# Kernel optimization log

Measured on AMD Instinct MI355X. Metric: run time of the kernel, lower is better.

## Reference

```python
import jax, jax.numpy as jnp
import numpy as np

B, QL, KVL = 2, 1024, 2048
D = 4096          # hidden_size
NH, NKV = 32, 8   # attention heads / kv heads
HD = D // NH      # head_dim = 128
INNER = 4 * D     # SwiGLU intermediate = 16384
EPS = 1e-5
THETA = 10000.0


def rope_cos_sin(seq_len, head_dim, theta):
    inv_freq = 1.0 / (theta ** (jnp.arange(0, head_dim, 2, dtype=jnp.float32) / head_dim))
    t = jnp.arange(seq_len, dtype=jnp.float32)
    freqs = jnp.outer(t, inv_freq)                      # [S, HD/2]
    emb = jnp.concatenate([freqs, freqs], axis=-1)      # [S, HD]
    return jnp.cos(emb), jnp.sin(emb)


def rotate_half(x):
    half = x.shape[-1] // 2
    return jnp.concatenate([-x[..., half:], x[..., :half]], axis=-1)


def apply_rope(x, cos, sin):
    # x: [B, H, S, HD]; cos/sin: [S, HD] broadcast over batch & heads
    return x * cos[None, None] + rotate_half(x) * sin[None, None]


def layernorm(x, w, b):
    mu = jnp.mean(x, axis=-1, keepdims=True)
    var = jnp.var(x, axis=-1, keepdims=True)
    return (x - mu) * jax.lax.rsqrt(var + EPS) * w + b


def setup_inputs() -> dict:
    key = jax.random.key(0)
    ks = jax.random.split(key, 12)
    s = 0.02
    return {
        "hidden_states": jax.random.normal(ks[0], (B, QL, D), jnp.float32),
        "encoder_hidden_states": jax.random.normal(ks[1], (B, KVL, D), jnp.float32),
        "encoder_attention_mask": jnp.ones((B, KVL), jnp.float32),
        "ln1_w": jnp.ones((D,), jnp.float32),
        "ln1_b": jnp.zeros((D,), jnp.float32),
        "q_w": jax.random.normal(ks[2], (D, D), jnp.float32) * s,        # [out, in]
        "k_w": jax.random.normal(ks[3], (NKV * HD, D), jnp.float32) * s,
        "v_w": jax.random.normal(ks[4], (NKV * HD, D), jnp.float32) * s,
        "o_w": jax.random.normal(ks[5], (D, D), jnp.float32) * s,
        "ln2_w": jnp.ones((D,), jnp.float32),
        "ln2_b": jnp.zeros((D,), jnp.float32),
        "gate_w": jax.random.normal(ks[6], (INNER, D), jnp.float32) * s,
        "up_w": jax.random.normal(ks[7], (INNER, D), jnp.float32) * s,
        "down_w": jax.random.normal(ks[8], (D, INNER), jnp.float32) * s,
    }


def reference(hidden_states, encoder_hidden_states, encoder_attention_mask,
              ln1_w, ln1_b, q_w, k_w, v_w, o_w, ln2_w, ln2_b,
              gate_w, up_w, down_w):
    residual = hidden_states
    h = layernorm(hidden_states, ln1_w, ln1_b)

    # projections
    q = (h @ q_w.T).reshape(B, QL, NH, HD).transpose(0, 2, 1, 3)                    # [B,NH,QL,HD]
    k = (encoder_hidden_states @ k_w.T).reshape(B, KVL, NKV, HD).transpose(0, 2, 1, 3)  # [B,NKV,KVL,HD]
    v = (encoder_hidden_states @ v_w.T).reshape(B, KVL, NKV, HD).transpose(0, 2, 1, 3)

    # RoPE: q uses positions 0..QL-1, k uses positions 0..KVL-1 (position_ids=None -> cos[None])
    q_cos, q_sin = rope_cos_sin(QL, HD, THETA)
    kv_cos, kv_sin = rope_cos_sin(KVL, HD, THETA)
    q = apply_rope(q, q_cos, q_sin)
    k = apply_rope(k, kv_cos, kv_sin)

    # GQA repeat_kv: each kv head repeated num_key_value_groups times consecutively
    n_rep = NH // NKV
    k = jnp.repeat(k, n_rep, axis=1)  # [B,NH,KVL,HD]
    v = jnp.repeat(v, n_rep, axis=1)

    attn = jnp.einsum('bhqd,bhkd->bhqk', q, k) / np.sqrt(HD).astype(np.float32)
    # NOTE: original code ADDS the boolean mask (True -> +1.0) to the logits
    mask = (encoder_attention_mask != 0).astype(attn.dtype)  # [B,KVL]
    attn = attn + mask[:, None, None, :]
    attn = jax.nn.softmax(attn.astype(jnp.float32), axis=-1).astype(q.dtype)

    out = jnp.einsum('bhqk,bhkd->bhqd', attn, v)        # [B,NH,QL,HD]
    out = out.transpose(0, 2, 1, 3).reshape(B, QL, D)
    attn_out = out @ o_w.T

    h = residual + attn_out
    residual = h
    h = layernorm(h, ln2_w, ln2_b)
    ff = (jax.nn.silu(h @ gate_w.T) * (h @ up_w.T)) @ down_w.T
    return residual + ff
```

## Files before the change

kernel.cpp:

```cpp
#include <hip/hip_runtime.h>
#include <hip/hip_bf16.h>
#include <math.h>

using bf16 = __hip_bfloat16;
typedef __bf16 bfv8 __attribute__((ext_vector_type(8)));
typedef float f32x4 __attribute__((ext_vector_type(4)));

__device__ __forceinline__ f32x4 mfma16(bfv8 a, bfv8 b, f32x4 c) {
    return __builtin_amdgcn_mfma_f32_16x16x32_bf16(a, b, c, 0, 0, 0);
}

__device__ __forceinline__ void gload_lds16(const void* g, void* l) {
    __builtin_amdgcn_global_load_lds(
        (const __attribute__((address_space(1))) void*)g,
        (__attribute__((address_space(3))) void*)l, 16, 0, 0);
}

__global__ void cvt_kernel(const float* __restrict__ in, bf16* __restrict__ out, long n8) {
    long u = (long)blockIdx.x * 256 + threadIdx.x;
    if (u >= n8) return;
    const float4* p = (const float4*)in + u * 2;
    float4 a = p[0], b = p[1];
    bf16 t8[8] = { __float2bfloat16(a.x), __float2bfloat16(a.y), __float2bfloat16(a.z), __float2bfloat16(a.w),
                   __float2bfloat16(b.x), __float2bfloat16(b.y), __float2bfloat16(b.z), __float2bfloat16(b.w) };
    *(int4*)(out + u * 8) = *(const int4*)t8;
}

__global__ void cvt2_kernel(const float* __restrict__ in1, bf16* __restrict__ out1,
                            const float* __restrict__ in2, bf16* __restrict__ out2, long n8) {
    long u = (long)blockIdx.x * 256 + threadIdx.x;
    const float* in = in1;
    bf16* out = out1;
    if (u >= n8) { u -= n8; in = in2; out = out2; }
    const float4* p = (const float4*)in + u * 2;
    float4 a = p[0], b = p[1];
    bf16 t8[8] = { __float2bfloat16(a.x), __float2bfloat16(a.y), __float2bfloat16(a.z), __float2bfloat16(a.w),
                   __float2bfloat16(b.x), __float2bfloat16(b.y), __float2bfloat16(b.z), __float2bfloat16(b.w) };
    *(int4*)(out + u * 8) = *(const int4*)t8;
}

__global__ void layernorm_kernel(const float* __restrict__ x, const float* __restrict__ gw,
                                 const float* __restrict__ gb, bf16* __restrict__ out)
{
    const int D = 4096;
    int row = blockIdx.x, t = threadIdx.x;
    const float4* xr = (const float4*)(x + (size_t)row * D);
    float4 v[4];
    float s1 = 0.f, s2 = 0.f;
#pragma unroll
    for (int j = 0; j < 4; ++j) {
        v[j] = xr[t + j * 256];
        s1 += v[j].x + v[j].y + v[j].z + v[j].w;
        s2 += v[j].x * v[j].x + v[j].y * v[j].y + v[j].z * v[j].z + v[j].w * v[j].w;
    }
#pragma unroll
    for (int d = 1; d < 64; d <<= 1) { s1 += __shfl_xor(s1, d); s2 += __shfl_xor(s2, d); }
    __shared__ float red[8];
    int wave = t >> 6, lane = t & 63;
    if (lane == 0) { red[wave] = s1; red[4 + wave] = s2; }
    __syncthreads();
    s1 = red[0] + red[1] + red[2] + red[3];
    s2 = red[4] + red[5] + red[6] + red[7];
    float mu = s1 * (1.f / 4096.f);
    float var = s2 * (1.f / 4096.f) - mu * mu;
    float rs = rsqrtf(var + 1e-5f);
    bf16* orow = out + (size_t)row * D;
#pragma unroll
    for (int j = 0; j < 4; ++j) {
        int base = (t + j * 256) * 4;
        float xs[4] = { v[j].x, v[j].y, v[j].z, v[j].w };
        bf16 o4[4];
#pragma unroll
        for (int c = 0; c < 4; ++c)
            o4[c] = __float2bfloat16((xs[c] - mu) * rs * gw[base + c] + gb[base + c]);
        *(int2*)(orow + base) = *(const int2*)o4;
    }
}

__global__ void rope_kernel(bf16* __restrict__ x, int nheads, int seqlen, long total) {
    long idx = (long)blockIdx.x * 256 + threadIdx.x;
    if (idx >= total) return;
    int j = (int)(idx & 63);
    long t2 = idx >> 6;
    int h = (int)(t2 % nheads);
    long row = t2 / nheads;
    int pos = (int)(row % seqlen);
    float inv = exp2f(-(float)j * 0.20762050593046015f);
    float ang = (float)pos * inv;
    float s, c;
    sincosf(ang, &s, &c);
    bf16* p = x + row * ((long)nheads * 128) + (long)h * 128 + j;
    float x0 = __bfloat162float(p[0]);
    float x1 = __bfloat162float(p[64]);
    p[0]  = __float2bfloat16(x0 * c - x1 * s);
    p[64] = __float2bfloat16(x1 * c + x0 * s);
}

template<int BM, int BN, int MODE, bool DUAL, int CM, int CN, int XN>
__global__ __launch_bounds__(512, 2) void gemm_p(
        const bf16* __restrict__ A, const bf16* __restrict__ W, const bf16* __restrict__ W2,
        void* __restrict__ Cout, void* __restrict__ Cout2, const void* __restrict__ aux,
        int M, int N, int K, int Nsplit)
{
    constexpr int MF = BM / 32;
    constexpr int NF = BN / 64;
    constexpr int ALD = BM / 128;
    constexpr int BLD = BN / 128;
    constexpr int SLD = ALD + BLD;
    __shared__ bf16 lds[3][(BM + BN) * 32];

    const int t = threadIdx.x;
    const int wid = t >> 6, lane = t & 63;
    const int lr = lane & 15, lg = lane >> 4;
    const int wr = wid >> 2, wc = wid & 3;
    const int bid = blockIdx.x;
    const int xcd = bid & 7, slot = bid >> 3;
    const int sm = slot / CN, sn = slot % CN;
    const int xm = xcd / XN, xn = xcd % XN;
    const int bm = (xm * CM + sm) * BM;
    const int bn = (xn * CN + sn) * BN;

    auto stage = [&](int tt, int buf) {
        const int k0 = tt * 32;
        char* ldsA = (char*)&lds[buf][0];
#pragma unroll
        for (int c = 0; c < ALD; ++c) {
            int Wb = (t + c * 512) * 16;
            int L = Wb ^ (((Wb >> 7) & 7) << 4);
            int row = L >> 6, colb = L & 63;
            gload_lds16(A + (size_t)(bm + row) * K + k0 + (colb >> 1), ldsA + Wb);
        }
        char* ldsB = (char*)&lds[buf][BM * 32];
#pragma unroll
        for (int c = 0; c < BLD; ++c) {
            int Wb = (t + c * 512) * 16;
            int L = Wb ^ (((Wb >> 7) & 7) << 4);
            int row = L >> 6, colb = L & 63;
            const bf16* src;
            if constexpr (DUAL) {
                int nr = bn + row;
                src = (nr >= Nsplit) ? W2 + (size_t)(nr - Nsplit) * K + k0 + (colb >> 1)
                                     : W  + (size_t)nr * K + k0 + (colb >> 1);
            } else {
                src = W + (size_t)(bn + row) * K + k0 + (colb >> 1);
            }
            gload_lds16(src, ldsB + Wb);
        }
    };

    const f32x4 zero4 = { 0.f, 0.f, 0.f, 0.f };
    f32x4 acc[MF][NF];
#pragma unroll
    for (int m = 0; m < MF; ++m)
#pragma unroll
        for (int n = 0; n < NF; ++n) acc[m][n] = zero4;

    const int T = K >> 5;
    stage(0, 0);
    stage(1, 1);
    if constexpr (SLD == 4) asm volatile("s_waitcnt vmcnt(4)" ::: "memory");
    else                    asm volatile("s_waitcnt vmcnt(3)" ::: "memory");
    __builtin_amdgcn_s_barrier();
    __builtin_amdgcn_sched_barrier(0);

    for (int tt = 0; tt < T; ++tt) {
        const int buf = tt % 3;
        bfv8 af[MF], bfr[NF];
#pragma unroll
        for (int m = 0; m < MF; ++m) {
            int row = wr * (BM / 2) + m * 16 + lr;
            int U = row * 64 + lg * 16;
            af[m] = *(const bfv8*)((const char*)&lds[buf][0] + (U ^ (((U >> 7) & 7) << 4)));
        }
#pragma unroll
        for (int n = 0; n < NF; ++n) {
            int row = wc * (BN / 4) + n * 16 + lr;
            int U = row * 64 + lg * 16;
            bfr[n] = *(const bfv8*)((const char*)&lds[buf][BM * 32] + (U ^ (((U >> 7) & 7) << 4)));
        }
        if (tt + 2 < T) stage(tt + 2, (tt + 2) % 3);
        __builtin_amdgcn_s_setprio(1);
#pragma unroll
        for (int m = 0; m < MF; ++m)
#pragma unroll
            for (int n = 0; n < NF; ++n)
                acc[m][n] = mfma16(af[m], bfr[n], acc[m][n]);
        __builtin_amdgcn_s_setprio(0);
        if (tt + 2 < T) {
            if constexpr (SLD == 4) asm volatile("s_waitcnt vmcnt(4)" ::: "memory");
            else                    asm volatile("s_waitcnt vmcnt(3)" ::: "memory");
        } else {
            asm volatile("s_waitcnt vmcnt(0)" ::: "memory");
        }
        __builtin_amdgcn_s_barrier();
        __builtin_amdgcn_sched_barrier(0);
    }

    const int r0 = bm + wr * (BM / 2), c0 = bn + wc * (BN / 4);
#pragma unroll
    for (int m = 0; m < MF; ++m)
#pragma unroll
        for (int n = 0; n < NF; ++n)
#pragma unroll
            for (int i = 0; i < 4; ++i) {
                int r = r0 + m * 16 + lg * 4 + i;
                int c = c0 + n * 16 + lr;
                float a = acc[m][n][i];
                if constexpr (DUAL) {
                    if (c < Nsplit) ((bf16*)Cout)[(size_t)r * Nsplit + c] = __float2bfloat16(a);
                    else ((bf16*)Cout2)[(size_t)r * (N - Nsplit) + (c - Nsplit)] = __float2bfloat16(a);
                } else {
                    size_t idx = (size_t)r * N + c;
                    if constexpr (MODE == 0) {
                        ((bf16*)Cout)[idx] = __float2bfloat16(a);
                    } else if constexpr (MODE == 1) {
                        a = a / (1.f + expf(-a));
                        ((bf16*)Cout)[idx] = __float2bfloat16(a);
                    } else if constexpr (MODE == 2) {
                        a *= __bfloat162float(((const bf16*)aux)[idx]);
                        ((bf16*)Cout)[idx] = __float2bfloat16(a);
                    } else {
                        ((float*)Cout)[idx] = a + ((const float*)aux)[idx];
                    }
                }
            }
}

template<int BN, int MODE, bool DUAL, int CM, int CN, int XN>
__global__ __launch_bounds__(512, 1) void gemm8(
        const bf16* __restrict__ A, const bf16* __restrict__ W, const bf16* __restrict__ W2,
        void* __restrict__ Cout, void* __restrict__ Cout2, const void* __restrict__ aux,
        int M, int N, int K, int Nsplit)
{
    constexpr bool BIG = (BN == 256);
    constexpr int NBUF = BIG ? 2 : 3;
    constexpr int ABY = 32768;
    constexpr int BBY = BN * 128;
    constexpr int TBY = ABY + BBY;
    __shared__ alignas(16) char lds8[NBUF * TBY];

    const int t = threadIdx.x;
    const int wid = t >> 6, lane = t & 63;
    const int lr = lane & 15, lg = lane >> 4;
    const int wrB = wid >> 2, wcB = wid & 3;
    const int wr4 = wid >> 1, wc4 = wid & 1;
    const int bid = blockIdx.x;
    const int xcd = bid & 7, slot = bid >> 3;
    const int sm = slot / CN, sn = slot % CN;
    const int xm = xcd / XN, xn = xcd % XN;
    const int bm = (xm * CM + sm) * 256;
    const int bn = (xn * CN + sn) * BN;

    auto stA = [&](int kt, int h, int buf) {
#pragma unroll
        for (int c = 0; c < 2; ++c) {
            int Wb = (t + c * 512) * 16;
            int L = Wb ^ (((Wb >> 7) & 7) << 4);
            gload_lds16(A + (size_t)(bm + h * 128 + (L >> 7)) * K + kt * 64 + ((L & 127) >> 1),
                        lds8 + buf * TBY + h * 16384 + Wb);
        }
    };
    auto stB = [&](int kt, int h, int buf) {
#pragma unroll
        for (int c = 0; c < 2; ++c) {
            int Wb = (t + c * 512) * 16;
            int L = Wb ^ (((Wb >> 7) & 7) << 4);
            int nr = bn + h * 128 + (L >> 7);
            const bf16* src;
            if constexpr (DUAL) {
                src = (nr >= Nsplit) ? W2 + (size_t)(nr - Nsplit) * K + kt * 64 + ((L & 127) >> 1)
                                     : W  + (size_t)nr * K + kt * 64 + ((L & 127) >> 1);
            } else {
                src = W + (size_t)nr * K + kt * 64 + ((L & 127) >> 1);
            }
            gload_lds16(src, lds8 + buf * TBY + ABY + h * 16384 + Wb);
        }
    };

    const f32x4 zero4 = { 0.f, 0.f, 0.f, 0.f };
    f32x4 acc[BIG ? 8 : 4][4];
#pragma unroll
    for (int m = 0; m < (BIG ? 8 : 4); ++m)
#pragma unroll
        for (int n = 0; n < 4; ++n) acc[m][n] = zero4;

    bfv8 af[4][2], bfr[2][2][2];
    bfv8 afs[2][2], bfs[4][2];

#define LOADA(BUF, MH) do {                                                   \
    const char* _ba = lds8 + (BUF) * TBY;                                     \
    _Pragma("unroll") for (int m = 0; m < 4; ++m)                             \
    _Pragma("unroll") for (int ks = 0; ks < 2; ++ks) {                        \
        int row = wrB * 128 + (MH) * 64 + m * 16 + lr;                        \
        int U = row * 128 + ks * 64 + lg * 16;                                \
        af[m][ks] = *(const bfv8*)(_ba + (U ^ ((row & 7) << 4)));             \
    } } while (0)

#define LOADB(BUF, NH) do {                                                   \
    const char* _bb = lds8 + (BUF) * TBY + ABY;                               \
    _Pragma("unroll") for (int n = 0; n < 2; ++n)                             \
    _Pragma("unroll") for (int ks = 0; ks < 2; ++ks) {                        \
        int row = wcB * 64 + (NH) * 32 + n * 16 + lr;                         \
        int U = row * 128 + ks * 64 + lg * 16;                                \
        bfr[NH][n][ks] = *(const bfv8*)(_bb + (U ^ ((row & 7) << 4)));        \
    } } while (0)

#define MFMAQ(MH, NH) do {                                                    \
    _Pragma("unroll") for (int m = 0; m < 4; ++m)                             \
    _Pragma("unroll") for (int n = 0; n < 2; ++n) {                           \
        acc[(MH)*4+m][(NH)*2+n] = mfma16(af[m][0], bfr[NH][n][0], acc[(MH)*4+m][(NH)*2+n]); \
        acc[(MH)*4+m][(NH)*2+n] = mfma16(af[m][1], bfr[NH][n][1], acc[(MH)*4+m][(NH)*2+n]); \
    } } while (0)

#define LOADA_S(BUF, MH) do {                                                 \
    const char* _ba = lds8 + (BUF) * TBY;                                     \
    _Pragma("unroll") for (int m = 0; m < 2; ++m)                             \
    _Pragma("unroll") for (int ks = 0; ks < 2; ++ks) {                        \
        int row = wr4 * 64 + (MH) * 32 + m * 16 + lr;                         \
        int U = row * 128 + ks * 64 + lg * 16;                                \
        afs[m][ks] = *(const bfv8*)(_ba + (U ^ ((row & 7) << 4)));            \
    } } while (0)

#define LOADB_S(BUF) do {                                                     \
    const char* _bb = lds8 + (BUF) * TBY + ABY;                               \
    _Pragma("unroll") for (int n = 0; n < 4; ++n)                             \
    _Pragma("unroll") for (int ks = 0; ks < 2; ++ks) {                        \
        int row = wc4 * 64 + n * 16 + lr;                                     \
        int U = row * 128 + ks * 64 + lg * 16;                                \
        bfs[n][ks] = *(const bfv8*)(_bb + (U ^ ((row & 7) << 4)));            \
    } } while (0)

#define MFMAQ_S(MH) do {                                                      \
    _Pragma("unroll") for (int m = 0; m < 2; ++m)                             \
    _Pragma("unroll") for (int n = 0; n < 4; ++n) {                           \
        acc[(MH)*2+m][n] = mfma16(afs[m][0], bfs[n][0], acc[(MH)*2+m][n]);    \
        acc[(MH)*2+m][n] = mfma16(afs[m][1], bfs[n][1], acc[(MH)*2+m][n]);    \
    } } while (0)

#define PH_TOP() do { __builtin_amdgcn_s_barrier();                           \
    asm volatile("s_waitcnt lgkmcnt(0)" ::: "memory");                        \
    __builtin_amdgcn_sched_barrier(0);                                        \
    __builtin_amdgcn_s_setprio(1); } while (0)

#define PH_END() do { __builtin_amdgcn_s_setprio(0);                          \
    __builtin_amdgcn_s_barrier(); } while (0)

#define GATE(LIVE) do { __builtin_amdgcn_s_setprio(0);                        \
    if (LIVE) { if constexpr (BIG) asm volatile("s_waitcnt vmcnt(4)" ::: "memory"); \
                else               asm volatile("s_waitcnt vmcnt(6)" ::: "memory"); } \
    else      asm volatile("s_waitcnt vmcnt(0)" ::: "memory");                \
    __builtin_amdgcn_s_barrier(); } while (0)

    const int T = K >> 6;
    const int T2 = T >> 1;

    if constexpr (BIG) {
        stA(0, 0, 0); stA(0, 1, 0); stB(0, 0, 0); stB(0, 1, 0);
        stB(1, 0, 1); stB(1, 1, 1);
        asm volatile("s_waitcnt vmcnt(4)" ::: "memory");
        __builtin_amdgcn_s_barrier();

        for (int tt = 0; tt < T2; ++tt) {
            const int o = 2 * tt + 1, e2 = 2 * tt + 2, o2 = 2 * tt + 3;
            const bool le = (e2 < T), lo = (o2 < T);
            LOADA(0, 0); LOADB(0, 0); stA(o, 0, 1);
            PH_TOP(); MFMAQ(0, 0); PH_END();
            LOADB(0, 1); stA(o, 1, 1);
            PH_TOP(); MFMAQ(0, 1); PH_END();
            LOADA(0, 1); if (le) stB(e2, 0, 0);
            PH_TOP(); MFMAQ(1, 1); PH_END();
            if (le) stB(e2, 1, 0);
            PH_TOP(); MFMAQ(1, 0); GATE(le);
            LOADA(1, 0); LOADB(1, 0); if (le) stA(e2, 0, 0);
            PH_TOP(); MFMAQ(0, 0); PH_END();
            LOADB(1, 1); if (le) stA(e2, 1, 0);
            PH_TOP(); MFMAQ(0, 1); PH_END();
            LOADA(1, 1); if (lo) stB(o2, 0, 1);
            PH_TOP(); MFMAQ(1, 1); PH_END();
            if (lo) stB(o2, 1, 1);
            PH_TOP(); MFMAQ(1, 0); GATE(le);
        }
    } else {
        stA(0, 0, 0); stB(0, 0, 0); stA(0, 1, 0);
        stA(1, 0, 1); stB(1, 0, 1); stA(1, 1, 1);
        asm volatile("s_waitcnt vmcnt(6)" ::: "memory");
        __builtin_amdgcn_s_barrier();

        int bE = 0, bO = 1, bN = 2;
        for (int tt = 0; tt < T2; ++tt) {
            const int e2 = 2 * tt + 2, o2 = 2 * tt + 3;
            const bool le = (e2 < T), lo = (o2 < T);
            LOADA_S(bE, 0); LOADB_S(bE); if (le) { stA(e2, 0, bN); stB(e2, 0, bN); }
            PH_TOP(); MFMAQ_S(0); PH_END();
            LOADA_S(bE, 1); if (le) stA(e2, 1, bN);
            PH_TOP(); MFMAQ_S(1); GATE(le);
            LOADA_S(bO, 0); LOADB_S(bO); if (lo) { stA(o2, 0, bE); stB(o2, 0, bE); }
            PH_TOP(); MFMAQ_S(0); PH_END();
            LOADA_S(bO, 1); if (lo) stA(o2, 1, bE);
            PH_TOP(); MFMAQ_S(1); GATE(lo);
            int nE = bN, nO = bE, nN = bO;
            bE = nE; bO = nO; bN = nN;
        }
    }

#undef LOADA
#undef LOADB
#undef MFMAQ
#undef LOADA_S
#undef LOADB_S
#undef MFMAQ_S
#undef PH_TOP
#undef PH_END
#undef GATE

    const int r0 = bm + (BIG ? wrB * 128 : wr4 * 64);
    const int c0 = bn + (BIG ? wcB * 64 : wc4 * 64);
#pragma unroll
    for (int mg = 0; mg < (BIG ? 8 : 4); ++mg)
#pragma unroll
        for (int ng = 0; ng < 4; ++ng)
#pragma unroll
            for (int i = 0; i < 4; ++i) {
                int r = r0 + mg * 16 + lg * 4 + i;
                int c = c0 + ng * 16 + lr;
                float a = acc[mg][ng][i];
                if constexpr (DUAL) {
                    if (c < Nsplit) ((bf16*)Cout)[(size_t)r * Nsplit + c] = __float2bfloat16(a);
                    else ((bf16*)Cout2)[(size_t)r * (N - Nsplit) + (c - Nsplit)] = __float2bfloat16(a);
                } else {
                    size_t idx = (size_t)r * N + c;
                    if constexpr (MODE == 0) {
                        ((bf16*)Cout)[idx] = __float2bfloat16(a);
                    } else if constexpr (MODE == 1) {
                        a = a / (1.f + expf(-a));
                        ((bf16*)Cout)[idx] = __float2bfloat16(a);
                    } else if constexpr (MODE == 2) {
                        a *= __bfloat162float(((const bf16*)aux)[idx]);
                        ((bf16*)Cout)[idx] = __float2bfloat16(a);
                    } else {
                        ((float*)Cout)[idx] = a + ((const float*)aux)[idx];
                    }
                }
            }
}

__global__ void transpose_v(const bf16* __restrict__ vb, bf16* __restrict__ vt) {
    __shared__ bf16 tile[64][68];
    int kv0 = blockIdx.x * 64, c0 = blockIdx.y * 64, b = blockIdx.z;
    int t = threadIdx.x;
    int cr = t & 15, rr = t >> 4;
#pragma unroll
    for (int j = 0; j < 4; ++j) {
        int r = rr + j * 16;
        *(int2*)&tile[r][cr * 4] = *(const int2*)&vb[(size_t)(b * 2048 + kv0 + r) * 1024 + c0 + cr * 4];
    }
    __syncthreads();
#pragma unroll
    for (int j = 0; j < 4; ++j) {
        int cc = rr + j * 16;
        bf16 tmp[4];
#pragma unroll
        for (int q = 0; q < 4; ++q) tmp[q] = tile[cr * 4 + q][cc];
        *(int2*)&vt[(size_t)(b * 1024 + c0 + cc) * 2048 + kv0 + cr * 4] = *(const int2*)tmp;
    }
}

__global__ __launch_bounds__(256) void attn_kernel(
    const bf16* __restrict__ Q, const bf16* __restrict__ Kb, const bf16* __restrict__ Vt,
    const float* __restrict__ mask, bf16* __restrict__ O)
{
    const int QL_ = 1024, KVL_ = 2048;
    const float scale = 0.08838834764831845f;
    int qt = blockIdx.x, h = blockIdx.y, b = blockIdx.z;
    int t = threadIdx.x, wave = t >> 6, lane = t & 63;
    int lr = lane & 15, lg = lane >> 4;
    int g = h >> 2;
    __shared__ bf16 Ksm[2][64 * 128];
    __shared__ bf16 Vsm[2][128 * 64];
    __shared__ bf16 Psm[4][16 * 72];
    int q0 = qt * 64 + wave * 16;

    auto stage = [&](int buf, int kv0) {
#pragma unroll
        for (int p2 = 0; p2 < 4; ++p2) {
            int Wb = (p2 * 256 + t) * 16;
            int row = Wb >> 8;
            int col = ((Wb & 255) ^ ((row & 7) << 4)) >> 1;
            gload_lds16(Kb + (size_t)(b * KVL_ + kv0 + row) * 1024 + g * 128 + col,
                        (char*)&Ksm[buf][0] + Wb);
        }
#pragma unroll
        for (int p2 = 0; p2 < 4; ++p2) {
            int Wb = (p2 * 256 + t) * 16;
            int row = Wb >> 7;
            int col = ((Wb & 127) ^ ((row & 7) << 4)) >> 1;
            gload_lds16(Vt + (size_t)(b * 1024 + g * 128 + row) * 2048 + kv0 + col,
                        (char*)&Vsm[buf][0] + Wb);
        }
    };

    const bf16* qptr = Q + (size_t)(b * QL_ + q0 + lr) * 4096 + h * 128;
    bfv8 qf[4];
#pragma unroll
    for (int kc = 0; kc < 4; ++kc) qf[kc] = *(const bfv8*)(qptr + kc * 32 + lg * 8);

    const f32x4 zero4 = { 0.f, 0.f, 0.f, 0.f };
    f32x4 accO[8];
#pragma unroll
    for (int dt = 0; dt < 8; ++dt) accO[dt] = zero4;
    float mrow[4] = { -1e30f, -1e30f, -1e30f, -1e30f };
    float lrow[4] = { 0.f, 0.f, 0.f, 0.f };

    stage(0, 0);
    int buf = 0;
    const int NT = KVL_ / 64;
    for (int tt = 0; tt < NT; ++tt) {
        const int kv0 = tt * 64;
        if (tt + 1 < NT) {
            stage(buf ^ 1, kv0 + 64);
            asm volatile("s_waitcnt vmcnt(8)" ::: "memory");
        } else {
            asm volatile("s_waitcnt vmcnt(0)" ::: "memory");
        }
        __builtin_amdgcn_s_barrier();

        f32x4 s[4];
#pragma unroll
        for (int ct = 0; ct < 4; ++ct) {
            s[ct] = zero4;
#pragma unroll
            for (int kc = 0; kc < 4; ++kc) {
                int row = ct * 16 + lr;
                int U = row * 256 + kc * 64 + lg * 16;
                bfv8 kf = *(const bfv8*)((const char*)&Ksm[buf][0] + (U ^ ((row & 7) << 4)));
                s[ct] = mfma16(qf[kc], kf, s[ct]);
            }
            float mv = mask[(size_t)b * KVL_ + kv0 + ct * 16 + lr];
            mv = (mv != 0.f) ? 1.f : 0.f;
#pragma unroll
            for (int i = 0; i < 4; ++i) s[ct][i] = s[ct][i] * scale + mv;
        }

        float rmx[4], mnew[4], corr[4], psum[4];
#pragma unroll
        for (int i = 0; i < 4; ++i) {
            rmx[i] = fmaxf(fmaxf(s[0][i], s[1][i]), fmaxf(s[2][i], s[3][i]));
#pragma unroll
            for (int d = 1; d < 16; d <<= 1) rmx[i] = fmaxf(rmx[i], __shfl_xor(rmx[i], d));
            mnew[i] = fmaxf(mrow[i], rmx[i]);
            corr[i] = expf(mrow[i] - mnew[i]);
            psum[i] = 0.f;
        }
#pragma unroll
        for (int ct = 0; ct < 4; ++ct)
#pragma unroll
            for (int i = 0; i < 4; ++i) {
                float pv = expf(s[ct][i] - mnew[i]);
                psum[i] += pv;
                Psm[wave][(lg * 4 + i) * 72 + ct * 16 + lr] = __float2bfloat16(pv);
            }
#pragma unroll
        for (int i = 0; i < 4; ++i) {
#pragma unroll
            for (int d = 1; d < 16; d <<= 1) psum[i] += __shfl_xor(psum[i], d);
            lrow[i] = lrow[i] * corr[i] + psum[i];
            mrow[i] = mnew[i];
        }
#pragma unroll
        for (int dt = 0; dt < 8; ++dt)
#pragma unroll
            for (int i = 0; i < 4; ++i) accO[dt][i] *= corr[i];

        bfv8 pf0 = *(const bfv8*)&Psm[wave][lr * 72 + 0 * 32 + lg * 8];
        bfv8 pf1 = *(const bfv8*)&Psm[wave][lr * 72 + 1 * 32 + lg * 8];
#pragma unroll
        for (int dt = 0; dt < 8; ++dt) {
            int row = dt * 16 + lr;
            int U0 = row * 128 + 0 * 64 + lg * 16;
            int U1 = row * 128 + 1 * 64 + lg * 16;
            bfv8 vf0 = *(const bfv8*)((const char*)&Vsm[buf][0] + (U0 ^ ((row & 7) << 4)));
            bfv8 vf1 = *(const bfv8*)((const char*)&Vsm[buf][0] + (U1 ^ ((row & 7) << 4)));
            accO[dt] = mfma16(pf0, vf0, accO[dt]);
            accO[dt] = mfma16(pf1, vf1, accO[dt]);
        }
        __builtin_amdgcn_s_barrier();
        buf ^= 1;
    }

    float invl[4];
#pragma unroll
    for (int i = 0; i < 4; ++i) invl[i] = 1.f / lrow[i];
#pragma unroll
    for (int dt = 0; dt < 8; ++dt)
#pragma unroll
        for (int i = 0; i < 4; ++i)
            O[(size_t)(b * QL_ + q0 + lg * 4 + i) * 4096 + h * 128 + dt * 16 + lr] =
                __float2bfloat16(accO[dt][i] * invl[i]);
}

extern "C" void kernel_launch(void* const* d_in, const int* in_sizes, int n_in,
                              void* d_out, int out_size, void* d_ws, size_t ws_size,
                              hipStream_t stream) {
    const float* hidden = (const float*)d_in[0];
    const float* enc    = (const float*)d_in[1];
    const float* mask   = (const float*)d_in[2];
    const float* ln1w   = (const float*)d_in[3];
    const float* ln1b   = (const float*)d_in[4];
    const float* qw     = (const float*)d_in[5];
    const float* kw     = (const float*)d_in[6];
    const float* vw     = (const float*)d_in[7];
    const float* ow     = (const float*)d_in[8];
    const float* ln2w   = (const float*)d_in[9];
    const float* ln2b   = (const float*)d_in[10];
    const float* gatew  = (const float*)d_in[11];
    const float* upw    = (const float*)d_in[12];
    const float* downw  = (const float*)d_in[13];
    float* out = (float*)d_out;
    char* ws = (char*)d_ws;

    bf16*  wbuf  = (bf16*)(ws);
    bf16*  wbuf2 = (bf16*)(ws + 8388608);
    bf16*  h1    = (bf16*)(ws + 134217728);
    bf16*  encb  = (bf16*)(ws + 150994944);
    bf16*  qb    = (bf16*)(ws + 184549376);
    bf16*  kb    = (bf16*)(ws + 201326592);
    bf16*  vb    = (bf16*)(ws + 209715200);
    bf16*  attno = (bf16*)(ws + 218103808);
    float* h2    = (float*)(ws + 234881024);
    bf16*  vt    = (bf16*)(ws + 234881024);
    bf16*  h2n   = (bf16*)(ws + 268435456);
    bf16*  g1    = (bf16*)(ws + 285212672);

    auto cvt = [&](const float* src, bf16* dst, long n) {
        cvt_kernel<<<(int)(n / 2048), 256, 0, stream>>>(src, dst, n / 8);
    };

    cvt(enc, encb, 16777216L);
    layernorm_kernel<<<2048, 256, 0, stream>>>(hidden, ln1w, ln1b, h1);

    cvt(qw, wbuf, 16777216L);
    gemm_p<128, 256, 0, false, 8, 4, 4><<<256, 512, 0, stream>>>(
        h1, wbuf, nullptr, qb, nullptr, nullptr, 2048, 4096, 4096, 0);
    rope_kernel<<<16384, 256, 0, stream>>>(qb, 32, 1024, 2048L * 32 * 64);

    cvt2_kernel<<<4096, 256, 0, stream>>>(kw, wbuf, vw, wbuf2, 524288L);
    gemm_p<128, 256, 0, true, 8, 4, 2><<<256, 512, 0, stream>>>(
        encb, wbuf, wbuf2, kb, vb, nullptr, 4096, 2048, 4096, 1024);
    rope_kernel<<<8192, 256, 0, stream>>>(kb, 8, 2048, 4096L * 8 * 64);
    transpose_v<<<dim3(32, 16, 2), 256, 0, stream>>>(vb, vt);

    attn_kernel<<<dim3(16, 32, 2), 256, 0, stream>>>(qb, kb, vt, mask, attno);

    cvt(ow, wbuf, 16777216L);
    gemm_p<128, 256, 3, false, 8, 4, 4><<<256, 512, 0, stream>>>(
        attno, wbuf, nullptr, h2, nullptr, hidden, 2048, 4096, 4096, 0);

    layernorm_kernel<<<2048, 256, 0, stream>>>(h2, ln2w, ln2b, h2n);

    cvt(gatew, wbuf, 67108864L);
    gemm8<256, 1, false, 8, 8, 8><<<512, 512, 0, stream>>>(
        h2n, wbuf, nullptr, g1, nullptr, nullptr, 2048, 16384, 4096, 0);
    cvt(upw, wbuf, 67108864L);
    gemm8<256, 2, false, 8, 8, 8><<<512, 512, 0, stream>>>(
        h2n, wbuf, nullptr, g1, nullptr, g1, 2048, 16384, 4096, 0);

    cvt(downw, wbuf, 67108864L);
    gemm8<128, 3, false, 8, 4, 8><<<256, 512, 0, stream>>>(
        g1, wbuf, nullptr, out, nullptr, h2, 2048, 4096, 16384, 0);
}
```

Baseline: 1.504 ms.

## Overlap weight fp32-to-bf16 conversions with GEMMs via extra converter blocks

Extends the projection GEMM kernel with extra blocks beyond the GEMM grid that convert upcoming weights (K/V, gate) from fp32 to bf16 while the GEMM tiles run, and merges the encoder and Q-weight conversions into one launch. A larger workspace layout keeps separate buffers so these conversions can run ahead without clobbering live data. The aim is to hide the memory-bound conversion passes and cut launch count. The converter blocks compete with GEMM blocks for CUs and bandwidth, and the path needs a larger workspace, falling back to the old schedule otherwise.

```diff
diff --git a/kernel.cpp b/kernel.cpp
--- a/kernel.cpp
+++ b/kernel.cpp
@@ -100,8 +100,30 @@
 __global__ __launch_bounds__(512, 2) void gemm_p(
         const bf16* __restrict__ A, const bf16* __restrict__ W, const bf16* __restrict__ W2,
         void* __restrict__ Cout, void* __restrict__ Cout2, const void* __restrict__ aux,
-        int M, int N, int K, int Nsplit)
+        int M, int N, int K, int Nsplit,
+        int ngemm, const float* __restrict__ cf1, bf16* __restrict__ cd1, long cn1,
+        const float* __restrict__ cf2, bf16* __restrict__ cd2, long cn2)
 {
+    const int t = threadIdx.x;
+    if ((int)blockIdx.x >= ngemm) {
+        const long nb = (long)gridDim.x - ngemm;
+        const long tot = cn1 + cn2;
+        for (long u = (long)((int)blockIdx.x - ngemm) * 512 + t; u < tot; u += nb * 512) {
+            const float* in = cf1;
+            bf16* op = cd1;
+            long v = u;
+            if (v >= cn1) { v -= cn1; in = cf2; op = cd2; }
+            float4 a = ((const float4*)in)[v * 2];
+            float4 b = ((const float4*)in)[v * 2 + 1];
+            bf16 t8[8] = { __float2bfloat16(a.x), __float2bfloat16(a.y),
+                           __float2bfloat16(a.z), __float2bfloat16(a.w),
+                           __float2bfloat16(b.x), __float2bfloat16(b.y),
+                           __float2bfloat16(b.z), __float2bfloat16(b.w) };
+            *(int4*)(op + v * 8) = *(const int4*)t8;
+        }
+        return;
+    }
+
     constexpr int MF = BM / 32;
     constexpr int NF = BN / 64;
     constexpr int ALD = BM / 128;
@@ -109,7 +131,6 @@
     constexpr int SLD = ALD + BLD;
     __shared__ bf16 lds[3][(BM + BN) * 32];
 
-    const int t = threadIdx.x;
     const int wid = t >> 6, lane = t & 63;
     const int lr = lane & 15, lg = lane >> 4;
     const int wr = wid >> 2, wc = wid & 3;
@@ -618,53 +639,107 @@
     float* out = (float*)d_out;
     char* ws = (char*)d_ws;
 
-    bf16*  wbuf  = (bf16*)(ws);
-    bf16*  wbuf2 = (bf16*)(ws + 8388608);
-    bf16*  h1    = (bf16*)(ws + 134217728);
-    bf16*  encb  = (bf16*)(ws + 150994944);
-    bf16*  qb    = (bf16*)(ws + 184549376);
-    bf16*  kb    = (bf16*)(ws + 201326592);
-    bf16*  vb    = (bf16*)(ws + 209715200);
-    bf16*  attno = (bf16*)(ws + 218103808);
-    float* h2    = (float*)(ws + 234881024);
-    bf16*  vt    = (bf16*)(ws + 234881024);
-    bf16*  h2n   = (bf16*)(ws + 268435456);
-    bf16*  g1    = (bf16*)(ws + 285212672);
-
     auto cvt = [&](const float* src, bf16* dst, long n) {
         cvt_kernel<<<(int)(n / 2048), 256, 0, stream>>>(src, dst, n / 8);
     };
 
-    cvt(enc, encb, 16777216L);
-    layernorm_kernel<<<2048, 256, 0, stream>>>(hidden, ln1w, ln1b, h1);
-
-    cvt(qw, wbuf, 16777216L);
-    gemm_p<128, 256, 0, false, 8, 4, 4><<<256, 512, 0, stream>>>(
-        h1, wbuf, nullptr, qb, nullptr, nullptr, 2048, 4096, 4096, 0);
-    rope_kernel<<<16384, 256, 0, stream>>>(qb, 32, 1024, 2048L * 32 * 64);
-
-    cvt2_kernel<<<4096, 256, 0, stream>>>(kw, wbuf, vw, wbuf2, 524288L);
-    gemm_p<128, 256, 0, true, 8, 4, 2><<<256, 512, 0, stream>>>(
-        encb, wbuf, wbuf2, kb, vb, nullptr, 4096, 2048, 4096, 1024);
-    rope_kernel<<<8192, 256, 0, stream>>>(kb, 8, 2048, 4096L * 8 * 64);
-    transpose_v<<<dim3(32, 16, 2), 256, 0, stream>>>(vb, vt);
-
-    attn_kernel<<<dim3(16, 32, 2), 256, 0, stream>>>(qb, kb, vt, mask, attno);
-
-    cvt(ow, wbuf, 16777216L);
-    gemm_p<128, 256, 3, false, 8, 4, 4><<<256, 512, 0, stream>>>(
-        attno, wbuf, nullptr, h2, nullptr, hidden, 2048, 4096, 4096, 0);
-
-    layernorm_kernel<<<2048, 256, 0, stream>>>(h2, ln2w, ln2b, h2n);
-
-    cvt(gatew, wbuf, 67108864L);
-    gemm8<256, 1, false, 8, 8, 8><<<512, 512, 0, stream>>>(
-        h2n, wbuf, nullptr, g1, nullptr, nullptr, 2048, 16384, 4096, 0);
-    cvt(upw, wbuf, 67108864L);
-    gemm8<256, 2, false, 8, 8, 8><<<512, 512, 0, stream>>>(
-        h2n, wbuf, nullptr, g1, nullptr, g1, 2048, 16384, 4096, 0);
-
-    cvt(downw, wbuf, 67108864L);
-    gemm8<128, 3, false, 8, 4, 8><<<256, 512, 0, stream>>>(
-        g1, wbuf, nullptr, out, nullptr, h2, 2048, 4096, 16384, 0);
-}
+    if (ws_size >= 385875968ULL) {
+        bf16* WA   = (bf16*)(ws);
+        bf16* h1   = (bf16*)(ws);
+        bf16* qwB  = (bf16*)(ws + 16777216);
+        bf16* kwB  = (bf16*)(ws + 50331648);
+        bf16* vwB  = (bf16*)(ws + 58720256);
+        bf16* WB   = (bf16*)(ws + 134217728);
+        bf16* encb = (bf16*)(ws + 134217728);
+        bf16* qb   = (bf16*)(ws + 167772160);
+        bf16* kb   = (bf16*)(ws + 184549376);
+        bf16* vb   = (bf16*)(ws + 192937984);
+        bf16* vt   = (bf16*)(ws + 201326592);
+        bf16* attno= (bf16*)(ws + 209715200);
+        bf16* owB  = (bf16*)(ws + 226492416);
+        float* h2  = (float*)(ws + 268435456);
+        bf16* h2n  = (bf16*)(ws + 301989888);
+        bf16* g1   = (bf16*)(ws + 318767104);
+
+        cvt2_kernel<<<16384, 256, 0, stream>>>(enc, encb, qw, qwB, 2097152L);
+        layernorm_kernel<<<2048, 256, 0, stream>>>(hidden, ln1w, ln1b, h1);
+
+        gemm_p<128, 256, 0, false, 8, 4, 4><<<384, 512, 0, stream>>>(
+            h1, qwB, nullptr, qb, nullptr, nullptr, 2048, 4096, 4096, 0,
+            256, kw, kwB, 524288L, vw, vwB, 524288L);
+        rope_kernel<<<16384, 256, 0, stream>>>(qb, 32, 1024, 2048L * 32 * 64);
+
+        gemm_p<128, 256, 0, true, 8, 4, 2><<<256, 512, 0, stream>>>(
+            encb, kwB, vwB, kb, vb, nullptr, 4096, 2048, 4096, 1024,
+            256, nullptr, nullptr, 0, nullptr, nullptr, 0);
+        rope_kernel<<<8192, 256, 0, stream>>>(kb, 8, 2048, 4096L * 8 * 64);
+        transpose_v<<<dim3(32, 16, 2), 256, 0, stream>>>(vb, vt);
+
+        attn_kernel<<<dim3(16, 32, 2), 256, 0, stream>>>(qb, kb, vt, mask, attno);
+
+        cvt(ow, owB, 16777216L);
+        gemm_p<128, 256, 3, false, 8, 4, 4><<<512, 512, 0, stream>>>(
+            attno, owB, nullptr, h2, nullptr, hidden, 2048, 4096, 4096, 0,
+            256, gatew, WA, 8388608L, nullptr, nullptr, 0);
+
+        layernorm_kernel<<<2048, 256, 0, stream>>>(h2, ln2w, ln2b, h2n);
+
+        gemm8<256, 1, false, 8, 8, 8><<<512, 512, 0, stream>>>(
+            h2n, WA, nullptr, g1, nullptr, nullptr, 2048, 16384, 4096, 0);
+        cvt(upw, WA, 67108864L);
+        gemm8<256, 2, false, 8, 8, 8><<<512, 512, 0, stream>>>(
+            h2n, WA, nullptr, g1, nullptr, g1, 2048, 16384, 4096, 0);
+        cvt(downw, WB, 67108864L);
+        gemm8<128, 3, false, 8, 4, 8><<<256, 512, 0, stream>>>(
+            g1, WB, nullptr, out, nullptr, h2, 2048, 4096, 16384, 0);
+    } else {
+        bf16*  wbuf  = (bf16*)(ws);
+        bf16*  wbuf2 = (bf16*)(ws + 8388608);
+        bf16*  h1    = (bf16*)(ws + 134217728);
+        bf16*  encb  = (bf16*)(ws + 150994944);
+        bf16*  qb    = (bf16*)(ws + 184549376);
+        bf16*  kb    = (bf16*)(ws + 201326592);
+        bf16*  vb    = (bf16*)(ws + 209715200);
+        bf16*  attno = (bf16*)(ws + 218103808);
+        float* h2    = (float*)(ws + 234881024);
+        bf16*  vt    = (bf16*)(ws + 234881024);
+        bf16*  h2n   = (bf16*)(ws + 268435456);
+        bf16*  g1    = (bf16*)(ws + 285212672);
+
+        cvt(enc, encb, 16777216L);
+        layernorm_kernel<<<2048, 256, 0, stream>>>(hidden, ln1w, ln1b, h1);
+
+        cvt(qw, wbuf, 16777216L);
+        gemm_p<128, 256, 0, false, 8, 4, 4><<<256, 512, 0, stream>>>(
+            h1, wbuf, nullptr, qb, nullptr, nullptr, 2048, 4096, 4096, 0,
+            256, nullptr, nullptr, 0, nullptr, nullptr, 0);
+        rope_kernel<<<16384, 256, 0, stream>>>(qb, 32, 1024, 2048L * 32 * 64);
+
+        cvt2_kernel<<<4096, 256, 0, stream>>>(kw, wbuf, vw, wbuf2, 524288L);
+        gemm_p<128, 256, 0, true, 8, 4, 2><<<256, 512, 0, stream>>>(
+            encb, wbuf, wbuf2, kb, vb, nullptr, 4096, 2048, 4096, 1024,
+            256, nullptr, nullptr, 0, nullptr, nullptr, 0);
+        rope_kernel<<<8192, 256, 0, stream>>>(kb, 8, 2048, 4096L * 8 * 64);
+        transpose_v<<<dim3(32, 16, 2), 256, 0, stream>>>(vb, vt);
+
+        attn_kernel<<<dim3(16, 32, 2), 256, 0, stream>>>(qb, kb, vt, mask, attno);
+
+        cvt(ow, wbuf, 16777216L);
+        gemm_p<128, 256, 3, false, 8, 4, 4><<<256, 512, 0, stream>>>(
+            attno, wbuf, nullptr, h2, nullptr, hidden, 2048, 4096, 4096, 0,
+            256, nullptr, nullptr, 0, nullptr, nullptr, 0);
+
+        layernorm_kernel<<<2048, 256, 0, stream>>>(h2, ln2w, ln2b, h2n);
+
+        cvt(gatew, wbuf, 67108864L);
+        gemm8<256, 1, false, 8, 8, 8><<<512, 512, 0, stream>>>(
+            h2n, wbuf, nullptr, g1, nullptr, nullptr, 2048, 16384, 4096, 0);
+        cvt(upw, wbuf, 67108864L);
+        gemm8<256, 2, false, 8, 8, 8><<<512, 512, 0, stream>>>(
+            h2n, wbuf, nullptr, g1, nullptr, g1, 2048, 16384, 4096, 0);
+
+        cvt(downw, wbuf, 67108864L);
+        gemm8<128, 3, false, 8, 4, 8><<<256, 512, 0, stream>>>(
+            g1, wbuf, nullptr, out, nullptr, h2, 2048, 4096, 16384, 0);
+    }
+}
```

Result: no change. 1.496 ms (median of 2 runs) (-0.5%).
